# Performance work log

Hardware: AMD Instinct MI355X
Metric: run time of the kernel (lower is better)

## Reference

```python
import jax, jax.numpy as jnp
import numpy as np

S, T, H, D = 4096, 4096, 16, 64
N_EMBD = H * D

def setup_inputs() -> dict:
    key = jax.random.key(0)
    kq, kk, kv, kw = jax.random.split(key, 4)
    q = jax.random.normal(kq, (S, H, D), dtype=jnp.float32)
    k = jax.random.normal(kk, (T, H, D), dtype=jnp.float32)
    v = jax.random.normal(kv, (T, H, D), dtype=jnp.float32)
    # GPT-2 style init: std = 0.02 / sqrt(2 * n_layer), n_layer = 24
    W_proj = jax.random.normal(kw, (N_EMBD, N_EMBD), dtype=jnp.float32) * (0.02 / np.sqrt(2 * 24))
    return {"q": q, "k": k, "v": v, "W_proj": W_proj}

def reference(q, k, v, W_proj):
    s, h, d = q.shape
    t = k.shape[0]
    # causal bias: mask positions where query index < key index (future keys)
    causal_bias = (jnp.arange(s)[:, None] < jnp.arange(t)[None, :]).astype(jnp.float32) * -10000.0
    scale = 1.0 / jnp.sqrt(jnp.float32(d))
    # [h, s, t] scores in fp32 (matches original .astype(jnp.float32))
    scores = jnp.einsum('shd,thd->hst', q, k).astype(jnp.float32) * scale + causal_bias
    attn = jax.nn.softmax(scores, axis=-1).astype(q.dtype)
    # dropout p=0 / inference -> identity
    out = jnp.einsum('hst,thd->shd', attn, v).reshape(s, h * d)
    # nn.Linear (no bias) vmapped over tokens: y = x @ W.T
    return out @ W_proj.T
```

## Files before the change

### kernel.cpp

```cpp
#include <hip/hip_runtime.h>

#define S_LEN 4096
#define NH 16
#define DH 64
#define NE 1024

typedef __bf16 bf16_t;
typedef __bf16 bf16x8 __attribute__((ext_vector_type(8)));
typedef __bf16 bf16x4 __attribute__((ext_vector_type(4)));
typedef __bf16 bf16x2 __attribute__((ext_vector_type(2)));
typedef float  f32x4  __attribute__((ext_vector_type(4)));

#define QSCALE 0.180336879f

__global__ __launch_bounds__(256) void pack_all(const float* __restrict__ q,
                                                const float* __restrict__ k,
                                                const float* __restrict__ w,
                                                const float* __restrict__ v,
                                                bf16_t* __restrict__ qb,
                                                bf16_t* __restrict__ kb,
                                                bf16_t* __restrict__ wb,
                                                bf16_t* __restrict__ vt) {
    __shared__ bf16_t tile[64][65];
    const int bid = blockIdx.x;
    if (bid < 4096) {
        const int tid = bid * 256 + threadIdx.x;
        const int e = tid * 4;
        const int s = e >> 10;
        const int c = e & (NE - 1);
        const int h = c >> 6;
        const int d = c & (DH - 1);
        const int o = (h * S_LEN + s) * DH + d;
        float4 qv = *(const float4*)(q + e);
        float4 kv = *(const float4*)(k + e);
        bf16x4 qo, ko;
        qo[0] = (bf16_t)(qv.x * QSCALE); qo[1] = (bf16_t)(qv.y * QSCALE);
        qo[2] = (bf16_t)(qv.z * QSCALE); qo[3] = (bf16_t)(qv.w * QSCALE);
        ko[0] = (bf16_t)kv.x; ko[1] = (bf16_t)kv.y; ko[2] = (bf16_t)kv.z; ko[3] = (bf16_t)kv.w;
        *(bf16x4*)(qb + o) = qo;
        *(bf16x4*)(kb + o) = ko;
        if (tid < (NE * NE / 4)) {
            float4 wv = *(const float4*)(w + tid * 4);
            bf16x4 wo;
            wo[0] = (bf16_t)wv.x; wo[1] = (bf16_t)wv.y; wo[2] = (bf16_t)wv.z; wo[3] = (bf16_t)wv.w;
            *(bf16x4*)(wb + tid * 4) = wo;
        }
    } else {
        const int vb = bid - 4096;
        const int h  = vb >> 6;
        const int t0 = (vb & 63) * 64;
        const int r  = threadIdx.x >> 6;
        const int cl = threadIdx.x & 63;
#pragma unroll
        for (int rep = 0; rep < 16; ++rep) {
            int i = rep * 4 + r;
            tile[cl][i] = (bf16_t)v[(t0 + i) * NE + h * DH + cl];
        }
        __syncthreads();
        const int r2  = threadIdx.x >> 5;
        const int cl2 = (threadIdx.x & 31) * 2;
#pragma unroll
        for (int rep = 0; rep < 8; ++rep) {
            int d = rep * 8 + r2;
            bf16x2 out;
            out[0] = tile[d][cl2];
            out[1] = tile[d][cl2 + 1];
            *(bf16x2*)(vt + (h * DH + d) * S_LEN + t0 + cl2) = out;
        }
    }
}

__global__ __launch_bounds__(512, 4) void attn(const bf16_t* __restrict__ qb,
                                               const bf16_t* __restrict__ kb,
                                               const bf16_t* __restrict__ vt,
                                               float* __restrict__ po,
                                               float* __restrict__ ls) {
    __shared__ __align__(16) bf16_t kbuf[2][64 * 72];
    __shared__ __align__(16) bf16_t vbuf[2][64 * 72];
    __shared__ __align__(16) bf16_t pbuf[8][16 * 72];

    const int tid  = threadIdx.x;
    const int wave = tid >> 6;
    const int lane = tid & 63;
    const int l15  = lane & 15;
    const int quad = lane >> 4;
    const int h = blockIdx.x;
    const int x = blockIdx.y;

    const int sA = x;
    const int sB = 31 - x;
    const int n0 = x + 1;
    const int b1 = sB + 1;
    const int N  = 33;

    const bf16_t* __restrict__ qh = qb + h * (S_LEN * DH);
    const bf16_t* __restrict__ kh = kb + h * (S_LEN * DH);
    const bf16_t* __restrict__ vh = vt + h * (DH * S_LEN);

    const int row0 = tid >> 3;
    const int tc8  = (tid & 7) * 8;

    f32x4 o_acc[4];
    float lsum[4];
    bf16x8 qA[2];
    int s0 = sA * 128 + wave * 16;

    auto load_q = [&](int s0_) {
#pragma unroll
        for (int dc = 0; dc < 2; ++dc)
            qA[dc] = *(const bf16x8*)(qh + (s0_ + l15) * DH + dc * 32 + quad * 8);
    };
    auto reset_acc = [&]() {
#pragma unroll
        for (int db = 0; db < 4; ++db) o_acc[db] = (f32x4){0.f, 0.f, 0.f, 0.f};
#pragma unroll
        for (int r = 0; r < 4; ++r) lsum[r] = 0.0f;
    };
    auto epilogue = [&](int s0_, int slot) {
        float l2[4];
#pragma unroll
        for (int r = 0; r < 4; ++r) l2[r] = lsum[r];
#pragma unroll
        for (int off = 8; off >= 1; off >>= 1)
#pragma unroll
            for (int r = 0; r < 4; ++r) l2[r] += __shfl_xor(l2[r], off, 64);
        float* poz = po + (size_t)(slot * NH + h) * S_LEN * DH;
#pragma unroll
        for (int db = 0; db < 4; ++db)
#pragma unroll
            for (int r = 0; r < 4; ++r)
                poz[(s0_ + quad * 4 + r) * DH + db * 16 + l15] = o_acc[db][r];
        if (l15 == 0) {
            float* lsz = ls + (size_t)(slot * NH + h) * S_LEN;
#pragma unroll
            for (int r = 0; r < 4; ++r) lsz[s0_ + quad * 4 + r] = l2[r];
        }
    };

    load_q(s0);
    reset_acc();

    {
        bf16x8 kr = *(const bf16x8*)(kh + row0 * DH + tc8);
        bf16x8 vr = *(const bf16x8*)(vh + row0 * S_LEN + tc8);
        *(bf16x8*)(kbuf[0] + row0 * 72 + tc8) = kr;
        *(bf16x8*)(vbuf[0] + row0 * 72 + tc8) = vr;
    }
    __syncthreads();

    for (int j = 0; j < N; ++j) {
        if (j == n0) {
            epilogue(s0, 0);
            s0 = sB * 128 + wave * 16;
            load_q(s0);
            reset_acc();
        }
        const int t0 = (j < n0 ? j : b1 + (j - n0)) * 64;
        const bf16_t* kb_ = kbuf[j & 1];
        const bf16_t* vb_ = vbuf[j & 1];

        bf16x8 krn, vrn;
        const bool pf = (j + 1 < N);
        if (pf) {
            const int jn = j + 1;
            const int tn = (jn < n0 ? jn : b1 + (jn - n0)) * 64;
            krn = *(const bf16x8*)(kh + (tn + row0) * DH + tc8);
            vrn = *(const bf16x8*)(vh + row0 * S_LEN + tn + tc8);
        }

        f32x4 c_[4];
#pragma unroll
        for (int ch = 0; ch < 4; ++ch) {
            bf16x8 kB0 = *(const bf16x8*)(kb_ + (ch * 16 + l15) * 72 + quad * 8);
            bf16x8 kB1 = *(const bf16x8*)(kb_ + (ch * 16 + l15) * 72 + 32 + quad * 8);
            f32x4 zr = (f32x4){0.f, 0.f, 0.f, 0.f};
            zr = __builtin_amdgcn_mfma_f32_16x16x32_bf16(qA[0], kB0, zr, 0, 0, 0);
            zr = __builtin_amdgcn_mfma_f32_16x16x32_bf16(qA[1], kB1, zr, 0, 0, 0);
            c_[ch] = zr;
        }

        if (t0 + 63 > s0) {
#pragma unroll
            for (int ch = 0; ch < 4; ++ch) {
                int col = t0 + ch * 16 + l15;
#pragma unroll
                for (int r = 0; r < 4; ++r) {
                    int row = s0 + quad * 4 + r;
                    if (col > row) c_[ch][r] = -INFINITY;
                }
            }
        }

        bf16_t* pl = pbuf[wave];
#pragma unroll
        for (int ch = 0; ch < 4; ++ch)
#pragma unroll
            for (int r = 0; r < 4; ++r) {
                float p = exp2f(c_[ch][r] - 17.0f);
                lsum[r] += p;
                pl[(quad * 4 + r) * 72 + ch * 16 + l15] = (bf16_t)p;
            }

        __builtin_amdgcn_wave_barrier();

        bf16x8 pA[2];
#pragma unroll
        for (int kc = 0; kc < 2; ++kc)
            pA[kc] = *(const bf16x8*)(pbuf[wave] + l15 * 72 + kc * 32 + quad * 8);

        bf16x8 vB[4][2];
#pragma unroll
        for (int db = 0; db < 4; ++db)
#pragma unroll
            for (int kc = 0; kc < 2; ++kc)
                vB[db][kc] = *(const bf16x8*)(vb_ + (db * 16 + l15) * 72 + kc * 32 + quad * 8);

#pragma unroll
        for (int db = 0; db < 4; ++db) {
            o_acc[db] = __builtin_amdgcn_mfma_f32_16x16x32_bf16(pA[0], vB[db][0], o_acc[db], 0, 0, 0);
            o_acc[db] = __builtin_amdgcn_mfma_f32_16x16x32_bf16(pA[1], vB[db][1], o_acc[db], 0, 0, 0);
        }

        if (pf) {
            *(bf16x8*)(kbuf[(j + 1) & 1] + row0 * 72 + tc8) = krn;
            *(bf16x8*)(vbuf[(j + 1) & 1] + row0 * 72 + tc8) = vrn;
        }
        __syncthreads();
    }

    epilogue(s0, 1);
}

__global__ __launch_bounds__(256) void combine(const float* __restrict__ po,
                                               const float* __restrict__ ls,
                                               bf16_t* __restrict__ xb) {
    const int idx = blockIdx.x * 256 + threadIdx.x;
    const int row = idx >> 8;
    const int c   = (idx & 255) * 4;
    const int h   = c >> 6;
    const int d   = c & 63;
    const size_t base0 = (size_t)(h) * S_LEN * DH + row * DH + d;
    const size_t base1 = (size_t)(NH + h) * S_LEN * DH + row * DH + d;
    float4 o0 = *(const float4*)(po + base0);
    float4 o1 = *(const float4*)(po + base1);
    float l = ls[(size_t)h * S_LEN + row] + ls[(size_t)(NH + h) * S_LEN + row];
    float inv = 1.0f / l;
    bf16x4 out;
    out[0] = (bf16_t)((o0.x + o1.x) * inv);
    out[1] = (bf16_t)((o0.y + o1.y) * inv);
    out[2] = (bf16_t)((o0.z + o1.z) * inv);
    out[3] = (bf16_t)((o0.w + o1.w) * inv);
    *(bf16x4*)(xb + (size_t)row * NE + c) = out;
}

__global__ __launch_bounds__(256, 4) void proj(const bf16_t* __restrict__ xb,
                                               const bf16_t* __restrict__ wb,
                                               float* __restrict__ y) {
    __shared__ __align__(16) bf16_t wbuf[2][64 * 72];
    const int tid  = threadIdx.x;
    const int wave = tid >> 6;
    const int lane = tid & 63;
    const int l15  = lane & 15;
    const int quad = lane >> 4;
    const int m0 = blockIdx.x * 64 + wave * 16;
    const int n0 = blockIdx.y * 64;

    const int row0 = tid >> 3;
    const int tc8  = (tid & 7) * 8;

    f32x4 acc[4];
#pragma unroll
    for (int nb = 0; nb < 4; ++nb) acc[nb] = (f32x4){0.f, 0.f, 0.f, 0.f};

    {
        bf16x8 wr0 = *(const bf16x8*)(wb + (n0 + row0) * NE + tc8);
        bf16x8 wr1 = *(const bf16x8*)(wb + (n0 + row0 + 32) * NE + tc8);
        *(bf16x8*)(wbuf[0] + row0 * 72 + tc8) = wr0;
        *(bf16x8*)(wbuf[0] + (row0 + 32) * 72 + tc8) = wr1;
    }
    bf16x8 a[2];
#pragma unroll
    for (int kc = 0; kc < 2; ++kc)
        a[kc] = *(const bf16x8*)(xb + (m0 + l15) * NE + kc * 32 + quad * 8);
    __syncthreads();

    for (int kt = 0; kt < 16; ++kt) {
        const bf16_t* wb_ = wbuf[kt & 1];
        const bool pf = (kt + 1 < 16);
        bf16x8 wr0, wr1, an[2];
        if (pf) {
            const int kn = (kt + 1) * 64;
            wr0 = *(const bf16x8*)(wb + (n0 + row0) * NE + kn + tc8);
            wr1 = *(const bf16x8*)(wb + (n0 + row0 + 32) * NE + kn + tc8);
#pragma unroll
            for (int kc = 0; kc < 2; ++kc)
                an[kc] = *(const bf16x8*)(xb + (m0 + l15) * NE + kn + kc * 32 + quad * 8);
        }

#pragma unroll
        for (int nb = 0; nb < 4; ++nb)
#pragma unroll
            for (int kc = 0; kc < 2; ++kc) {
                bf16x8 b = *(const bf16x8*)(wb_ + (nb * 16 + l15) * 72 + kc * 32 + quad * 8);
                acc[nb] = __builtin_amdgcn_mfma_f32_16x16x32_bf16(a[kc], b, acc[nb], 0, 0, 0);
            }

        if (pf) {
            *(bf16x8*)(wbuf[(kt + 1) & 1] + row0 * 72 + tc8) = wr0;
            *(bf16x8*)(wbuf[(kt + 1) & 1] + (row0 + 32) * 72 + tc8) = wr1;
#pragma unroll
            for (int kc = 0; kc < 2; ++kc) a[kc] = an[kc];
        }
        __syncthreads();
    }

#pragma unroll
    for (int nb = 0; nb < 4; ++nb)
#pragma unroll
        for (int r = 0; r < 4; ++r)
            y[(m0 + quad * 4 + r) * NE + n0 + nb * 16 + l15] = acc[nb][r];
}

extern "C" void kernel_launch(void* const* d_in, const int* in_sizes, int n_in,
                              void* d_out, int out_size, void* d_ws, size_t ws_size,
                              hipStream_t stream) {
    const float* q = (const float*)d_in[0];
    const float* k = (const float*)d_in[1];
    const float* v = (const float*)d_in[2];
    const float* w = (const float*)d_in[3];
    float* y = (float*)d_out;

    bf16_t* ws = (bf16_t*)d_ws;
    bf16_t* qb = ws;
    bf16_t* kb = qb + 4 * 1024 * 1024;
    bf16_t* vt = kb + 4 * 1024 * 1024;
    bf16_t* wb = vt + 4 * 1024 * 1024;
    bf16_t* xb = wb + 1024 * 1024;
    float*  po = (float*)(xb + 4 * 1024 * 1024);
    float*  ls = po + (size_t)2 * NH * S_LEN * DH;

    pack_all<<<dim3(4096 + 1024), dim3(256), 0, stream>>>(q, k, w, v, qb, kb, wb, vt);
    attn<<<dim3(NH, 32), dim3(512), 0, stream>>>(qb, kb, vt, po, ls);
    combine<<<dim3(4096), dim3(256), 0, stream>>>(po, ls, xb);
    proj<<<dim3(S_LEN / 64, NE / 64), dim3(256), 0, stream>>>(xb, wb, y);
}
```

Before: 198.5 us.

## Split causal attention into 256-row query blocks with 4-way KV splits

Each attention block now holds 16 waves and covers 256 query rows, so every K/V tile loaded into LDS is shared by twice as many query rows. The causal work is balanced by pairing query blocks p and 15-p and splitting the combined KV range into four 17-tile chunks. The combine kernel sums up to four partials per row instead of two. The row sums are now computed with an MFMA against a ones vector rather than scalar adds followed by shuffles, and K and V loads are divided between the two halves of the block. In exchange the kernel uses more partial-output workspace and does more combine traffic, and 1024-thread blocks with launch_bounds(1024, 8) may cap registers per thread.

```diff
diff --git a/kernel.cpp b/kernel.cpp
--- a/kernel.cpp
+++ b/kernel.cpp
@@ -70,14 +70,14 @@
     }
 }
 
-__global__ __launch_bounds__(512, 4) void attn(const bf16_t* __restrict__ qb,
-                                               const bf16_t* __restrict__ kb,
-                                               const bf16_t* __restrict__ vt,
-                                               float* __restrict__ po,
-                                               float* __restrict__ ls) {
+__global__ __launch_bounds__(1024, 8) void attn(const bf16_t* __restrict__ qb,
+                                                const bf16_t* __restrict__ kb,
+                                                const bf16_t* __restrict__ vt,
+                                                float* __restrict__ po,
+                                                float* __restrict__ ls) {
     __shared__ __align__(16) bf16_t kbuf[2][64 * 72];
     __shared__ __align__(16) bf16_t vbuf[2][64 * 72];
-    __shared__ __align__(16) bf16_t pbuf[8][16 * 72];
+    __shared__ __align__(16) bf16_t pbuf[16][16 * 72];
 
     const int tid  = threadIdx.x;
     const int wave = tid >> 6;
@@ -86,24 +86,36 @@
     const int quad = lane >> 4;
     const int h = blockIdx.x;
     const int x = blockIdx.y;
-
-    const int sA = x;
-    const int sB = 31 - x;
-    const int n0 = x + 1;
-    const int b1 = sB + 1;
-    const int N  = 33;
+    const int p = x >> 2;
+    const int b = x & 3;
+
+    const int ns   = 4 * p + 4;
+    const int vbeg = 17 * b;
+    int n0 = ns - vbeg;
+    n0 = n0 < 0 ? 0 : (n0 > 17 ? 17 : n0);
 
     const bf16_t* __restrict__ qh = qb + h * (S_LEN * DH);
     const bf16_t* __restrict__ kh = kb + h * (S_LEN * DH);
     const bf16_t* __restrict__ vh = vt + h * (DH * S_LEN);
 
-    const int row0 = tid >> 3;
-    const int tc8  = (tid & 7) * 8;
+    const int half = tid >> 9;
+    const int idx  = tid & 511;
+    const int row0 = idx >> 3;
+    const int tc8  = (idx & 7) * 8;
+    const bf16_t* sbase = half ? (vh + row0 * S_LEN + tc8) : (kh + row0 * 64 + tc8);
+    const int tstep = half ? 64 : 4096;
+    bf16_t* dst0 = (half ? vbuf[0] : kbuf[0]) + row0 * 72 + tc8;
+    bf16_t* dst1 = (half ? vbuf[1] : kbuf[1]) + row0 * 72 + tc8;
 
     f32x4 o_acc[4];
-    float lsum[4];
+    f32x4 lacc;
     bf16x8 qA[2];
-    int s0 = sA * 128 + wave * 16;
+    int s0 = (n0 > 0 ? p * 256 : (15 - p) * 256) + wave * 16;
+
+    const bf16_t onev = (l15 == 0) ? (bf16_t)1.0f : (bf16_t)0.0f;
+    bf16x8 bOnes;
+#pragma unroll
+    for (int j = 0; j < 8; ++j) bOnes[j] = onev;
 
     auto load_q = [&](int s0_) {
 #pragma unroll
@@ -113,27 +125,19 @@
     auto reset_acc = [&]() {
 #pragma unroll
         for (int db = 0; db < 4; ++db) o_acc[db] = (f32x4){0.f, 0.f, 0.f, 0.f};
-#pragma unroll
-        for (int r = 0; r < 4; ++r) lsum[r] = 0.0f;
+        lacc = (f32x4){0.f, 0.f, 0.f, 0.f};
     };
-    auto epilogue = [&](int s0_, int slot) {
-        float l2[4];
-#pragma unroll
-        for (int r = 0; r < 4; ++r) l2[r] = lsum[r];
-#pragma unroll
-        for (int off = 8; off >= 1; off >>= 1)
-#pragma unroll
-            for (int r = 0; r < 4; ++r) l2[r] += __shfl_xor(l2[r], off, 64);
-        float* poz = po + (size_t)(slot * NH + h) * S_LEN * DH;
+    auto epilogue = [&](int s0_) {
+        float* poz = po + (size_t)(b * NH + h) * S_LEN * DH;
 #pragma unroll
         for (int db = 0; db < 4; ++db)
 #pragma unroll
             for (int r = 0; r < 4; ++r)
                 poz[(s0_ + quad * 4 + r) * DH + db * 16 + l15] = o_acc[db][r];
         if (l15 == 0) {
-            float* lsz = ls + (size_t)(slot * NH + h) * S_LEN;
-#pragma unroll
-            for (int r = 0; r < 4; ++r) lsz[s0_ + quad * 4 + r] = l2[r];
+            float* lsz = ls + (size_t)(b * NH + h) * S_LEN;
+#pragma unroll
+            for (int r = 0; r < 4; ++r) lsz[s0_ + quad * 4 + r] = lacc[r];
         }
     };
 
@@ -141,31 +145,29 @@
     reset_acc();
 
     {
-        bf16x8 kr = *(const bf16x8*)(kh + row0 * DH + tc8);
-        bf16x8 vr = *(const bf16x8*)(vh + row0 * S_LEN + tc8);
-        *(bf16x8*)(kbuf[0] + row0 * 72 + tc8) = kr;
-        *(bf16x8*)(vbuf[0] + row0 * 72 + tc8) = vr;
+        const int t = (0 < n0) ? vbeg : vbeg - ns;
+        bf16x8 r = *(const bf16x8*)(sbase + t * tstep);
+        *(bf16x8*)dst0 = r;
     }
     __syncthreads();
 
-    for (int j = 0; j < N; ++j) {
-        if (j == n0) {
-            epilogue(s0, 0);
-            s0 = sB * 128 + wave * 16;
+    for (int j = 0; j < 17; ++j) {
+        if (j == n0 && n0 > 0 && n0 < 17) {
+            epilogue(s0);
+            s0 = (15 - p) * 256 + wave * 16;
             load_q(s0);
             reset_acc();
         }
-        const int t0 = (j < n0 ? j : b1 + (j - n0)) * 64;
+        const int t  = (j < n0) ? vbeg + j : vbeg + j - ns;
+        const int t0 = t * 64;
         const bf16_t* kb_ = kbuf[j & 1];
         const bf16_t* vb_ = vbuf[j & 1];
 
-        bf16x8 krn, vrn;
-        const bool pf = (j + 1 < N);
+        bf16x8 stg;
+        const bool pf = (j + 1 < 17);
         if (pf) {
-            const int jn = j + 1;
-            const int tn = (jn < n0 ? jn : b1 + (jn - n0)) * 64;
-            krn = *(const bf16x8*)(kh + (tn + row0) * DH + tc8);
-            vrn = *(const bf16x8*)(vh + row0 * S_LEN + tn + tc8);
+            const int tn = (j + 1 < n0) ? vbeg + j + 1 : vbeg + j + 1 - ns;
+            stg = *(const bf16x8*)(sbase + tn * tstep);
         }
 
         f32x4 c_[4];
@@ -196,9 +198,8 @@
         for (int ch = 0; ch < 4; ++ch)
 #pragma unroll
             for (int r = 0; r < 4; ++r) {
-                float p = exp2f(c_[ch][r] - 17.0f);
-                lsum[r] += p;
-                pl[(quad * 4 + r) * 72 + ch * 16 + l15] = (bf16_t)p;
+                float pv = exp2f(c_[ch][r] - 17.0f);
+                pl[(quad * 4 + r) * 72 + ch * 16 + l15] = (bf16_t)pv;
             }
 
         __builtin_amdgcn_wave_barrier();
@@ -220,36 +221,46 @@
             o_acc[db] = __builtin_amdgcn_mfma_f32_16x16x32_bf16(pA[0], vB[db][0], o_acc[db], 0, 0, 0);
             o_acc[db] = __builtin_amdgcn_mfma_f32_16x16x32_bf16(pA[1], vB[db][1], o_acc[db], 0, 0, 0);
         }
+        lacc = __builtin_amdgcn_mfma_f32_16x16x32_bf16(pA[0], bOnes, lacc, 0, 0, 0);
+        lacc = __builtin_amdgcn_mfma_f32_16x16x32_bf16(pA[1], bOnes, lacc, 0, 0, 0);
 
         if (pf) {
-            *(bf16x8*)(kbuf[(j + 1) & 1] + row0 * 72 + tc8) = krn;
-            *(bf16x8*)(vbuf[(j + 1) & 1] + row0 * 72 + tc8) = vrn;
+            *(bf16x8*)((j & 1) ? dst0 : dst1) = stg;
         }
         __syncthreads();
     }
 
-    epilogue(s0, 1);
+    epilogue(s0);
 }
 
 __global__ __launch_bounds__(256) void combine(const float* __restrict__ po,
                                                const float* __restrict__ ls,
                                                bf16_t* __restrict__ xb) {
-    const int idx = blockIdx.x * 256 + threadIdx.x;
-    const int row = idx >> 8;
-    const int c   = (idx & 255) * 4;
+    const int row = blockIdx.x;
+    const int c   = threadIdx.x * 4;
     const int h   = c >> 6;
     const int d   = c & 63;
-    const size_t base0 = (size_t)(h) * S_LEN * DH + row * DH + d;
-    const size_t base1 = (size_t)(NH + h) * S_LEN * DH + row * DH + d;
-    float4 o0 = *(const float4*)(po + base0);
-    float4 o1 = *(const float4*)(po + base1);
-    float l = ls[(size_t)h * S_LEN + row] + ls[(size_t)(NH + h) * S_LEN + row];
+    const int sig = row >> 8;
+    const int p   = (sig < 8) ? sig : 15 - sig;
+    const int ns  = 4 * p + 4;
+    int b_lo, b_hi;
+    if (sig < 8) { b_lo = 0; b_hi = (ns + 16) / 17; }
+    else         { b_lo = ns / 17; b_hi = 4; }
+
+    float4 o = {0.f, 0.f, 0.f, 0.f};
+    float l = 0.f;
+    for (int bb = b_lo; bb < b_hi; ++bb) {
+        const float* poz = po + ((size_t)(bb * NH + h) * S_LEN + row) * DH + d;
+        float4 t = *(const float4*)poz;
+        o.x += t.x; o.y += t.y; o.z += t.z; o.w += t.w;
+        l += ls[(size_t)(bb * NH + h) * S_LEN + row];
+    }
     float inv = 1.0f / l;
     bf16x4 out;
-    out[0] = (bf16_t)((o0.x + o1.x) * inv);
-    out[1] = (bf16_t)((o0.y + o1.y) * inv);
-    out[2] = (bf16_t)((o0.z + o1.z) * inv);
-    out[3] = (bf16_t)((o0.w + o1.w) * inv);
+    out[0] = (bf16_t)(o.x * inv);
+    out[1] = (bf16_t)(o.y * inv);
+    out[2] = (bf16_t)(o.z * inv);
+    out[3] = (bf16_t)(o.w * inv);
     *(bf16x4*)(xb + (size_t)row * NE + c) = out;
 }
 
@@ -301,8 +312,8 @@
         for (int nb = 0; nb < 4; ++nb)
 #pragma unroll
             for (int kc = 0; kc < 2; ++kc) {
-                bf16x8 b = *(const bf16x8*)(wb_ + (nb * 16 + l15) * 72 + kc * 32 + quad * 8);
-                acc[nb] = __builtin_amdgcn_mfma_f32_16x16x32_bf16(a[kc], b, acc[nb], 0, 0, 0);
+                bf16x8 bfrag = *(const bf16x8*)(wb_ + (nb * 16 + l15) * 72 + kc * 32 + quad * 8);
+                acc[nb] = __builtin_amdgcn_mfma_f32_16x16x32_bf16(a[kc], bfrag, acc[nb], 0, 0, 0);
             }
 
         if (pf) {
@@ -337,10 +348,10 @@
     bf16_t* wb = vt + 4 * 1024 * 1024;
     bf16_t* xb = wb + 1024 * 1024;
     float*  po = (float*)(xb + 4 * 1024 * 1024);
-    float*  ls = po + (size_t)2 * NH * S_LEN * DH;
+    float*  ls = po + (size_t)4 * NH * S_LEN * DH;
 
     pack_all<<<dim3(4096 + 1024), dim3(256), 0, stream>>>(q, k, w, v, qb, kb, wb, vt);
-    attn<<<dim3(NH, 32), dim3(512), 0, stream>>>(qb, kb, vt, po, ls);
+    attn<<<dim3(NH, 32), dim3(1024), 0, stream>>>(qb, kb, vt, po, ls);
     combine<<<dim3(4096), dim3(256), 0, stream>>>(po, ls, xb);
     proj<<<dim3(S_LEN / 64, NE / 64), dim3(256), 0, stream>>>(xb, wb, y);
 }
```

Result: slower. 216.7 us (+9.2%).
